# Performance work log

Hardware: AMD Instinct MI355X
Metric: run time of the kernel (lower is better)

## Reference

```python
import jax, jax.numpy as jnp
import numpy as np

H = 16  # num_attention_heads
D = 64  # attention_head_size


def setup_inputs() -> dict:
    key = jax.random.key(0)
    ks = jax.random.split(key, 10)
    B, S, Hid = 8, 512, 1024
    scale = 0.02
    hidden_states = jax.random.normal(ks[0], (B, S, Hid), jnp.float32)
    attention_mask = jnp.zeros((B, 1, 1, S), jnp.float32)
    graph_emb = jax.random.randint(ks[1], (B, S, S), 0, 3, jnp.int32)
    Wq = jax.random.normal(ks[2], (Hid, Hid), jnp.float32) * scale
    bq = jnp.zeros((Hid,), jnp.float32)
    Wk = jax.random.normal(ks[3], (Hid, Hid), jnp.float32) * scale
    bk = jnp.zeros((Hid,), jnp.float32)
    Wv = jax.random.normal(ks[4], (Hid, Hid), jnp.float32) * scale
    bv = jnp.zeros((Hid,), jnp.float32)
    dp_k = jax.random.normal(ks[5], (3, D), jnp.float32) * scale
    dp_v = jax.random.normal(ks[6], (3, D), jnp.float32) * scale
    return {"hidden_states": hidden_states, "attention_mask": attention_mask,
            "graph_emb": graph_emb, "Wq": Wq, "bq": bq, "Wk": Wk, "bk": bk,
            "Wv": Wv, "bv": bv, "dp_k": dp_k, "dp_v": dp_v}


def reference(hidden_states, attention_mask, graph_emb, Wq, bq, Wk, bk, Wv, bv, dp_k, dp_v):
    B, S, Hid = hidden_states.shape

    def proj(W, b):  # nn.Linear: x @ W.T + b, then split heads -> [B,H,S,D]
        y = hidden_states @ W.T + b
        return y.reshape(B, S, H, D).transpose(0, 2, 1, 3)

    q = proj(Wq, bq)
    k = proj(Wk, bk)
    v = proj(Wv, bv)

    # padding_idx=0 -> row 0 of relation tables is zero
    dp_k = dp_k.at[0].set(0.0)
    dp_v = dp_v.at[0].set(0.0)
    dp_keys = dp_k[graph_emb]    # [B,S,S,D]
    dp_values = dp_v[graph_emb]  # [B,S,S,D]

    scores = jnp.einsum('bhqd,bhkd->bhqk', q, k) / jnp.sqrt(jnp.float32(D))
    scores = scores + jnp.einsum('bhqd,bqkd->bhqk', q, dp_keys)  # relative_matmul_dp
    scores = scores + attention_mask
    probs = jax.nn.softmax(scores, axis=-1)

    ctx = jnp.einsum('bhqk,bhkd->bhqd', probs, v)
    ctx = ctx + jnp.einsum('bhqk,bqkd->bhqd', probs, dp_values)  # relative_matmul_dpv
    return ctx.transpose(0, 2, 1, 3).reshape(B, S, H * D)
```

## Files before the change

### kernel.cpp

```cpp
#include <hip/hip_runtime.h>
#include <hip/hip_bf16.h>
#include <cstddef>

#define B_  8
#define S_  512
#define HID 1024
#define H_  16
#define D_  64

typedef float f32x4 __attribute__((ext_vector_type(4)));
typedef _Float16 f16x8 __attribute__((ext_vector_type(8)));
typedef short s16x8 __attribute__((ext_vector_type(8)));
typedef unsigned short u16t;

__device__ __forceinline__ u16t f2h(float v) {
    return __builtin_bit_cast(u16t, (_Float16)v);
}
__device__ __forceinline__ float h2f(u16t u) {
    return (float)__builtin_bit_cast(_Float16, u);
}

__device__ __forceinline__ void gll16(const u16t* g, u16t* l) {
    __builtin_amdgcn_global_load_lds(
        (const __attribute__((address_space(1))) unsigned int*)(const void*)g,
        (__attribute__((address_space(3))) unsigned int*)(void*)l, 16, 0, 0);
}

__global__ __launch_bounds__(256) void conv_all_kernel(
    const float* __restrict__ X,
    const float* __restrict__ Wq, const float* __restrict__ Wk,
    const float* __restrict__ Wv,
    u16t* __restrict__ Xh, u16t* __restrict__ Wh)
{
    const int nX4 = (B_ * S_ * HID) / 4;
    const int nW4 = (HID * HID) / 4;
    int i = blockIdx.x * 256 + threadIdx.x;
    const float* src;
    u16t* dst;
    int off;
    if (i < nX4)                { src = X;  dst = Xh;                         off = i; }
    else if (i < nX4 + nW4)     { src = Wq; dst = Wh;                         off = i - nX4; }
    else if (i < nX4 + 2 * nW4) { src = Wk; dst = Wh + (size_t)HID * HID;     off = i - nX4 - nW4; }
    else                        { src = Wv; dst = Wh + (size_t)2 * HID * HID; off = i - nX4 - 2 * nW4; }
    float4 x = ((const float4*)src)[off];
    ushort4 h;
    h.x = f2h(x.x);
    h.y = f2h(x.y);
    h.z = f2h(x.z);
    h.w = f2h(x.w);
    ((ushort4*)dst)[off] = h;
}

__global__ __launch_bounds__(256) void qkv_mfma_kernel(
    const u16t* __restrict__ Xhi, const u16t* __restrict__ Whi,
    const float* __restrict__ bq, const float* __restrict__ bk,
    const float* __restrict__ bv,
    u16t* __restrict__ Qh, u16t* __restrict__ Kh, u16t* __restrict__ Vth)
{
    const int which = blockIdx.z;
    const u16t* __restrict__ WhiB = Whi + (size_t)which * (HID * HID);
    const float* __restrict__ bias = (which == 0) ? bq : (which == 1) ? bk : bv;

    __shared__ __align__(16) u16t SM[2 * 16384];

    const int tid  = threadIdx.x;
    const int lane = tid & 63;
    const int wv_  = tid >> 6;
    const int wr   = wv_ >> 1;
    const int wc   = wv_ & 1;
    const int m0   = blockIdx.y * 128;
    const int n0   = blockIdx.x * 128;

    f32x4 acc[4][4];
    #pragma unroll
    for (int mi = 0; mi < 4; ++mi)
        #pragma unroll
        for (int ni = 0; ni < 4; ++ni)
            #pragma unroll
            for (int e = 0; e < 4; ++e) acc[mi][ni][e] = 0.0f;

    const int rowB0 = wv_ * 32 + (lane >> 3);
    const int ch    = (lane & 7) ^ (rowB0 & 7);
    const size_t aof = (size_t)(m0 + rowB0) * HID + ch * 8;
    const size_t bof = (size_t)(n0 + rowB0) * HID + ch * 8;
    const int ldsA = (wv_ * 32) * 64;

    const int colL = lane & 15;
    const int kg   = lane >> 4;
    const int sx   = colL & 7;
    const int arow = (wr * 64 + colL) * 64;
    const int brow = (wc * 64 + colL) * 64;

    #pragma unroll
    for (int s = 0; s < 4; ++s) {
        gll16(&Xhi [aof + (size_t)(s * 8) * HID], SM + ldsA + s * 512);
        gll16(&WhiB[bof + (size_t)(s * 8) * HID], SM + 8192 + ldsA + s * 512);
    }
    __syncthreads();

    for (int k0 = 0; k0 < HID; k0 += 64) {
        const int cur = (k0 >> 6) & 1;
        u16t* const bufc = SM + cur * 16384;
        if (k0 + 64 < HID) {
            u16t* const bufn = SM + (cur ^ 1) * 16384;
            #pragma unroll
            for (int s = 0; s < 4; ++s) {
                gll16(&Xhi [aof + k0 + 64 + (size_t)(s * 8) * HID], bufn + ldsA + s * 512);
                gll16(&WhiB[bof + k0 + 64 + (size_t)(s * 8) * HID], bufn + 8192 + ldsA + s * 512);
            }
        }

        #pragma unroll
        for (int ks = 0; ks < 2; ++ks) {
            const int so = ((ks * 4 + kg) ^ sx) * 8;
            f16x8 a_[4], b_[4];
            #pragma unroll
            for (int mi = 0; mi < 4; ++mi)
                a_[mi] = *(const f16x8*)&bufc[arow + mi * 1024 + so];
            #pragma unroll
            for (int ni = 0; ni < 4; ++ni)
                b_[ni] = *(const f16x8*)&bufc[8192 + brow + ni * 1024 + so];
            #pragma unroll
            for (int mi = 0; mi < 4; ++mi)
                #pragma unroll
                for (int ni = 0; ni < 4; ++ni)
                    acc[mi][ni] = __builtin_amdgcn_mfma_f32_16x16x32_f16(
                        a_[mi], b_[ni], acc[mi][ni], 0, 0, 0);
        }
        __syncthreads();
    }

    if (which == 2) {
        #pragma unroll
        for (int mi = 0; mi < 4; ++mi) {
            #pragma unroll
            for (int ni = 0; ni < 4; ++ni) {
                const int n    = n0 + wc * 64 + ni * 16 + colL;
                const int mrow = m0 + wr * 64 + mi * 16 + kg * 4;
                const float bn = bias[n];
                const int bb = mrow >> 9;
                const int ss = mrow & (S_ - 1);
                const int hh = n >> 6;
                const int dd = n & (D_ - 1);
                ushort4 vh;
                vh.x = f2h(acc[mi][ni][0] + bn);
                vh.y = f2h(acc[mi][ni][1] + bn);
                vh.z = f2h(acc[mi][ni][2] + bn);
                vh.w = f2h(acc[mi][ni][3] + bn);
                *(ushort4*)&Vth[(((size_t)bb * H_ + hh) * D_ + dd) * S_ + ss] = vh;
            }
        }
    } else {
        u16t* __restrict__ Oh = (which == 0) ? Qh : Kh;
        float* LF = (float*)SM;
        float bn4[4];
        #pragma unroll
        for (int ni = 0; ni < 4; ++ni) bn4[ni] = bias[n0 + wc * 64 + ni * 16 + colL];

        const int er  = tid >> 3;
        const int ecc = (tid & 7) * 16;
        const int ehh = (n0 + ecc) >> 6;
        const int edd = ecc & 63;
        const int mrowE = m0 + (er >> 4) * 64 + (er & 15);

        #pragma unroll
        for (int mi = 0; mi < 4; ++mi) {
            __syncthreads();
            #pragma unroll
            for (int ni = 0; ni < 4; ++ni)
                #pragma unroll
                for (int j = 0; j < 4; ++j)
                    LF[(wr * 16 + kg * 4 + j) * 130 + wc * 64 + ni * 16 + colL] =
                        acc[mi][ni][j] + bn4[ni];
            __syncthreads();

            const int mrow = mrowE + mi * 16;
            const int bb = mrow >> 9;
            const int ss = mrow & (S_ - 1);
            __align__(16) u16t hv[16];
            #pragma unroll
            for (int u = 0; u < 16; u += 4) {
                float4 v = *(const float4*)&LF[er * 130 + ecc + u];
                hv[u + 0] = f2h(v.x);
                hv[u + 1] = f2h(v.y);
                hv[u + 2] = f2h(v.z);
                hv[u + 3] = f2h(v.w);
            }
            const size_t off = (((size_t)bb * H_ + ehh) * S_ + ss) * D_ + edd;
            *(s16x8*)&Oh[off]     = *(const s16x8*)&hv[0];
            *(s16x8*)&Oh[off + 8] = *(const s16x8*)&hv[8];
        }
    }
}

__global__ __launch_bounds__(512) void attn_mfma_kernel(
    const u16t* __restrict__ Qhg, const u16t* __restrict__ Khg,
    const u16t* __restrict__ Vhg,
    const int*  __restrict__ ge,  const float* __restrict__ mask,
    const float* __restrict__ dpk, const float* __restrict__ dpv,
    float* __restrict__ out)
{
    __shared__ __align__(16) u16t Q_s[128 * 64];
    __shared__ __align__(16) u16t K_s[64 * 64];
    __shared__ __align__(16) u16t V_s[64 * 64];
    __shared__ __align__(16) u16t P_s[8 * 2304];

    const int tid  = threadIdx.x;
    const int lane = tid & 63;
    const int wq   = tid >> 6;
    const int c    = lane & 15;
    const int g    = lane >> 4;
    const int sx   = c & 7;
    const int bid  = blockIdx.x;
    const int bh   = bid >> 2;
    const int q0   = (bid & 3) * 128;
    const int b    = bh >> 4;
    const int h    = bh & (H_ - 1);

    u16t* Pw = &P_s[wq * 2304];

    {
        const u16t* qbase = Qhg + ((size_t)bh * S_ + q0) * D_;
        #pragma unroll
        for (int t = 0; t < 2; ++t) {
            const int chk = tid + t * 512;
            const int r = chk >> 3, s = chk & 7;
            *(s16x8*)&Q_s[r * 64 + ((s ^ (r & 7)) << 3)] =
                *(const s16x8*)&qbase[chk * 8];
        }
    }

    const int r_   = tid >> 3;
    const int s_   = tid & 7;
    const int ldso = r_ * 64 + ((s_ ^ (r_ & 7)) << 3);
    const u16t* kgp = &Khg[((size_t)bh * S_ + r_) * D_ + s_ * 8];
    const u16t* vgp = &Vhg[((size_t)bh * D_ + r_) * S_ + s_ * 8];

    {
        s16x8 kr = *(const s16x8*)kgp;
        s16x8 vr = *(const s16x8*)vgp;
        *(s16x8*)&K_s[ldso] = kr;
        *(s16x8*)&V_s[ldso] = vr;
    }
    __syncthreads();

    float tq1, tq2;
    {
        const int qrow = wq * 16 + c;
        float a1 = 0.f, a2 = 0.f;
        #pragma unroll
        for (int t = 0; t < 2; ++t) {
            const int slot = 2 * g + t;
            const f16x8 qv8 = *(const f16x8*)&Q_s[qrow * 64 + ((slot ^ sx) << 3)];
            const int dbase = slot * 8;
            #pragma unroll
            for (int i = 0; i < 8; ++i) {
                const float qv = (float)qv8[i];
                a1 = fmaf(qv, dpk[D_ + dbase + i], a1);
                a2 = fmaf(qv, dpk[2 * D_ + dbase + i], a2);
            }
        }
        a1 += __shfl_xor(a1, 16); a1 += __shfl_xor(a1, 32);
        a2 += __shfl_xor(a2, 16); a2 += __shfl_xor(a2, 32);
        tq1 = a1; tq2 = a2;
    }

    const size_t geoff = ((size_t)b * S_ + q0 + wq * 16 + c) * S_;
    const float* mrow = &mask[(size_t)b * S_];

    float mrun = -INFINITY, lrun = 0.f, w1 = 0.f, w2 = 0.f;
    f32x4 ctx4[4];
    #pragma unroll
    for (int mi = 0; mi < 4; ++mi)
        #pragma unroll
        for (int e = 0; e < 4; ++e) ctx4[mi][e] = 0.f;

    for (int kt = 0; kt < S_ / 64; ++kt) {
        const int k0 = kt * 64;

        s16x8 krB, vrB;
        if (kt < S_ / 64 - 1) {
            krB = *(const s16x8*)(kgp + (size_t)(k0 + 64) * D_);
            vrB = *(const s16x8*)(vgp + (k0 + 64));
        }
        int4   gc4[4];
        float4 mk4[4];
        #pragma unroll
        for (int mi = 0; mi < 4; ++mi) {
            gc4[mi] = *(const int4*)&ge[geoff + k0 + mi * 16 + g * 4];
            mk4[mi] = *(const float4*)&mrow[k0 + mi * 16 + g * 4];
        }

        f32x4 s4[4];
        #pragma unroll
        for (int mi = 0; mi < 4; ++mi)
            #pragma unroll
            for (int e = 0; e < 4; ++e) s4[mi][e] = 0.f;

        __builtin_amdgcn_s_setprio(1);
        #pragma unroll
        for (int ks = 0; ks < 2; ++ks) {
            const int so = ((g + 4 * ks) ^ sx) << 3;
            const f16x8 qh_ = *(const f16x8*)&Q_s[(wq * 16 + c) * 64 + so];
            #pragma unroll
            for (int mi = 0; mi < 4; ++mi) {
                const f16x8 kh_ = *(const f16x8*)&K_s[(mi * 16 + c) * 64 + so];
                s4[mi] = __builtin_amdgcn_mfma_f32_16x16x32_f16(kh_, qh_, s4[mi], 0, 0, 0);
            }
        }
        __builtin_amdgcn_s_setprio(0);

        float sv[4][4];
        int   gcode[4][4];
        float tmax = -INFINITY;
        #pragma unroll
        for (int mi = 0; mi < 4; ++mi) {
            const int   gg[4] = {gc4[mi].x, gc4[mi].y, gc4[mi].z, gc4[mi].w};
            const float mm[4] = {mk4[mi].x, mk4[mi].y, mk4[mi].z, mk4[mi].w};
            #pragma unroll
            for (int j = 0; j < 4; ++j) {
                const float t = (gg[j] == 1) ? tq1 : (gg[j] == 2) ? tq2 : 0.f;
                const float x = fmaf(s4[mi][j], 0.125f, t + mm[j]);
                sv[mi][j] = x;
                gcode[mi][j] = gg[j];
                tmax = fmaxf(tmax, x);
            }
        }
        tmax = fmaxf(tmax, __shfl_xor(tmax, 16));
        tmax = fmaxf(tmax, __shfl_xor(tmax, 32));

        if (!__all(tmax - mrun <= 8.0f)) {
            const float mn    = fmaxf(mrun, tmax);
            const float alpha = __expf(mrun - mn);
            mrun = mn;
            lrun *= alpha; w1 *= alpha; w2 *= alpha;
            #pragma unroll
            for (int mi = 0; mi < 4; ++mi) ctx4[mi] *= alpha;
        }

        float rs = 0.f, rb1 = 0.f, rb2 = 0.f;
        #pragma unroll
        for (int mi = 0; mi < 4; ++mi)
            #pragma unroll
            for (int j = 0; j < 4; ++j) {
                const float e = __expf(sv[mi][j] - mrun);
                sv[mi][j] = e;
                rs += e;
                rb1 += (gcode[mi][j] == 1) ? e : 0.f;
                rb2 += (gcode[mi][j] == 2) ? e : 0.f;
            }
        rs  += __shfl_xor(rs, 16);  rs  += __shfl_xor(rs, 32);
        rb1 += __shfl_xor(rb1, 16); rb1 += __shfl_xor(rb1, 32);
        rb2 += __shfl_xor(rb2, 16); rb2 += __shfl_xor(rb2, 32);

        lrun += rs;
        w1   += rb1;
        w2   += rb2;

        #pragma unroll
        for (int mi = 0; mi < 4; ++mi) {
            ushort4 ph;
            ph.x = f2h(sv[mi][0]);
            ph.y = f2h(sv[mi][1]);
            ph.z = f2h(sv[mi][2]);
            ph.w = f2h(sv[mi][3]);
            const int slotp = (2 * mi + (g >> 1)) ^ sx;
            *(ushort4*)&Pw[c * 64 + slotp * 8 + (g & 1) * 4] = ph;
        }

        __builtin_amdgcn_s_setprio(1);
        #pragma unroll
        for (int ks = 0; ks < 2; ++ks) {
            const int so = ((g + 4 * ks) ^ sx) << 3;
            const f16x8 ph_ = *(const f16x8*)&Pw[c * 64 + so];
            #pragma unroll
            for (int mi = 0; mi < 4; ++mi) {
                const f16x8 vh_ = *(const f16x8*)&V_s[(mi * 16 + c) * 64 + so];
                ctx4[mi] = __builtin_amdgcn_mfma_f32_16x16x32_f16(vh_, ph_, ctx4[mi], 0, 0, 0);
            }
        }
        __builtin_amdgcn_s_setprio(0);
        __syncthreads();

        if (kt < S_ / 64 - 1) {
            *(s16x8*)&K_s[ldso] = krB;
            *(s16x8*)&V_s[ldso] = vrB;
            __syncthreads();
        }
    }

    const float inv = 1.0f / lrun;
    float* tb = (float*)&P_s[wq * 2304];
    #pragma unroll
    for (int mi = 0; mi < 4; ++mi) {
        const float4 dk1 = *(const float4*)&dpv[D_ + mi * 16 + g * 4];
        const float4 dk2 = *(const float4*)&dpv[2 * D_ + mi * 16 + g * 4];
        const float a1[4] = {dk1.x, dk1.y, dk1.z, dk1.w};
        const float a2[4] = {dk2.x, dk2.y, dk2.z, dk2.w};
        #pragma unroll
        for (int j = 0; j < 4; ++j) {
            const float val = (ctx4[mi][j] + w1 * a1[j] + w2 * a2[j]) * inv;
            tb[(mi * 16 + g * 4 + j) * 17 + c] = val;
        }
    }
    __syncthreads();
    #pragma unroll
    for (int qq = 0; qq < 16; ++qq)
        out[((size_t)b * S_ + q0 + wq * 16 + qq) * (H_ * D_) + h * D_ + lane] =
            tb[lane * 17 + qq];
}

extern "C" void kernel_launch(void* const* d_in, const int* in_sizes, int n_in,
                              void* d_out, int out_size, void* d_ws, size_t ws_size,
                              hipStream_t stream)
{
    const float* hs   = (const float*)d_in[0];
    const float* mask = (const float*)d_in[1];
    const int*   ge   = (const int*)d_in[2];
    const float* Wq   = (const float*)d_in[3];
    const float* bq   = (const float*)d_in[4];
    const float* Wk   = (const float*)d_in[5];
    const float* bk   = (const float*)d_in[6];
    const float* Wv   = (const float*)d_in[7];
    const float* bv   = (const float*)d_in[8];
    const float* dpk  = (const float*)d_in[9];
    const float* dpv  = (const float*)d_in[10];
    float* out = (float*)d_out;

    const size_t per = (size_t)B_ * H_ * S_ * D_;
    const size_t nX  = (size_t)B_ * S_ * HID;
    const size_t nW  = (size_t)HID * HID;

    u16t* base = (u16t*)d_ws;
    u16t* Qh  = base;
    u16t* Kh  = Qh  + per;
    u16t* Vth = Kh  + per;
    u16t* Xhi = Vth + per;
    u16t* Whi = Xhi + nX;

    const int nConv = (int)((nX + 3 * nW) / 4);
    conv_all_kernel<<<nConv / 256, 256, 0, stream>>>(hs, Wq, Wk, Wv, Xhi, Whi);

    dim3 gridG(HID / 128, (B_ * S_) / 128, 3);
    qkv_mfma_kernel<<<gridG, dim3(256), 0, stream>>>(
        Xhi, Whi, bq, bk, bv, Qh, Kh, Vth);

    dim3 gridB(B_ * H_ * (S_ / 128));
    attn_mfma_kernel<<<gridB, dim3(512), 0, stream>>>(
        Qh, Kh, Vth, ge, mask, dpk, dpv, out);
}
```

Before: 79.65 us.

## Keep Q in registers and double-buffer K/V tiles with one barrier per step

Q fragments are loaded straight from global memory into registers, so the Q tile no longer needs to be staged in LDS. K/V tiles are now double-buffered in a single shared array. Each iteration stores the prefetched tile into the alternate buffer before one __syncthreads, instead of a trailing barrier plus a store and a second barrier. Per-wave P scratch shrinks and LDS use drops substantially, which may allow more resident blocks per CU, at the cost of some extra registers for the held Q fragments.

```diff
diff --git a/kernel.cpp b/kernel.cpp
--- a/kernel.cpp
+++ b/kernel.cpp
@@ -200,10 +200,7 @@
     const float* __restrict__ dpk, const float* __restrict__ dpv,
     float* __restrict__ out)
 {
-    __shared__ __align__(16) u16t Q_s[128 * 64];
-    __shared__ __align__(16) u16t K_s[64 * 64];
-    __shared__ __align__(16) u16t V_s[64 * 64];
-    __shared__ __align__(16) u16t P_s[8 * 2304];
+    __shared__ __align__(16) u16t SM[24576];
 
     const int tid  = threadIdx.x;
     const int lane = tid & 63;
@@ -217,17 +214,28 @@
     const int b    = bh >> 4;
     const int h    = bh & (H_ - 1);
 
-    u16t* Pw = &P_s[wq * 2304];
-
+    u16t* Pw = SM + 16384 + wq * 1024;
+
+    const int qrow = q0 + wq * 16 + c;
+    const size_t qoff = ((size_t)bh * S_ + qrow) * D_;
+    const f16x8 qA = *(const f16x8*)&Qhg[qoff + g * 8];
+    const f16x8 qB = *(const f16x8*)&Qhg[qoff + (g + 4) * 8];
+
+    float tq1, tq2;
     {
-        const u16t* qbase = Qhg + ((size_t)bh * S_ + q0) * D_;
-        #pragma unroll
-        for (int t = 0; t < 2; ++t) {
-            const int chk = tid + t * 512;
-            const int r = chk >> 3, s = chk & 7;
-            *(s16x8*)&Q_s[r * 64 + ((s ^ (r & 7)) << 3)] =
-                *(const s16x8*)&qbase[chk * 8];
-        }
+        float a1 = 0.f, a2 = 0.f;
+        #pragma unroll
+        for (int i = 0; i < 8; ++i) {
+            const float x0 = (float)qA[i];
+            const float x1 = (float)qB[i];
+            a1 = fmaf(x0, dpk[D_ + g * 8 + i], a1);
+            a1 = fmaf(x1, dpk[D_ + (g + 4) * 8 + i], a1);
+            a2 = fmaf(x0, dpk[2 * D_ + g * 8 + i], a2);
+            a2 = fmaf(x1, dpk[2 * D_ + (g + 4) * 8 + i], a2);
+        }
+        a1 += __shfl_xor(a1, 16); a1 += __shfl_xor(a1, 32);
+        a2 += __shfl_xor(a2, 16); a2 += __shfl_xor(a2, 32);
+        tq1 = a1; tq2 = a2;
     }
 
     const int r_   = tid >> 3;
@@ -236,36 +244,10 @@
     const u16t* kgp = &Khg[((size_t)bh * S_ + r_) * D_ + s_ * 8];
     const u16t* vgp = &Vhg[((size_t)bh * D_ + r_) * S_ + s_ * 8];
 
-    {
-        s16x8 kr = *(const s16x8*)kgp;
-        s16x8 vr = *(const s16x8*)vgp;
-        *(s16x8*)&K_s[ldso] = kr;
-        *(s16x8*)&V_s[ldso] = vr;
-    }
-    __syncthreads();
-
-    float tq1, tq2;
-    {
-        const int qrow = wq * 16 + c;
-        float a1 = 0.f, a2 = 0.f;
-        #pragma unroll
-        for (int t = 0; t < 2; ++t) {
-            const int slot = 2 * g + t;
-            const f16x8 qv8 = *(const f16x8*)&Q_s[qrow * 64 + ((slot ^ sx) << 3)];
-            const int dbase = slot * 8;
-            #pragma unroll
-            for (int i = 0; i < 8; ++i) {
-                const float qv = (float)qv8[i];
-                a1 = fmaf(qv, dpk[D_ + dbase + i], a1);
-                a2 = fmaf(qv, dpk[2 * D_ + dbase + i], a2);
-            }
-        }
-        a1 += __shfl_xor(a1, 16); a1 += __shfl_xor(a1, 32);
-        a2 += __shfl_xor(a2, 16); a2 += __shfl_xor(a2, 32);
-        tq1 = a1; tq2 = a2;
-    }
-
-    const size_t geoff = ((size_t)b * S_ + q0 + wq * 16 + c) * S_;
+    s16x8 krS = *(const s16x8*)kgp;
+    s16x8 vrS = *(const s16x8*)vgp;
+
+    const size_t geoff = ((size_t)b * S_ + qrow) * S_;
     const float* mrow = &mask[(size_t)b * S_];
 
     float mrun = -INFINITY, lrun = 0.f, w1 = 0.f, w2 = 0.f;
@@ -277,11 +259,16 @@
 
     for (int kt = 0; kt < S_ / 64; ++kt) {
         const int k0 = kt * 64;
-
-        s16x8 krB, vrB;
+        const int bufo = (kt & 1) << 13;
+        u16t* const Kb = SM + bufo;
+        u16t* const Vb = SM + bufo + 4096;
+
+        *(s16x8*)&Kb[ldso] = krS;
+        *(s16x8*)&Vb[ldso] = vrS;
+
         if (kt < S_ / 64 - 1) {
-            krB = *(const s16x8*)(kgp + (size_t)(k0 + 64) * D_);
-            vrB = *(const s16x8*)(vgp + (k0 + 64));
+            krS = *(const s16x8*)(kgp + (size_t)(k0 + 64) * D_);
+            vrS = *(const s16x8*)(vgp + (k0 + 64));
         }
         int4   gc4[4];
         float4 mk4[4];
@@ -291,6 +278,8 @@
             mk4[mi] = *(const float4*)&mrow[k0 + mi * 16 + g * 4];
         }
 
+        __syncthreads();
+
         f32x4 s4[4];
         #pragma unroll
         for (int mi = 0; mi < 4; ++mi)
@@ -301,10 +290,10 @@
         #pragma unroll
         for (int ks = 0; ks < 2; ++ks) {
             const int so = ((g + 4 * ks) ^ sx) << 3;
-            const f16x8 qh_ = *(const f16x8*)&Q_s[(wq * 16 + c) * 64 + so];
+            const f16x8 qh_ = ks ? qB : qA;
             #pragma unroll
             for (int mi = 0; mi < 4; ++mi) {
-                const f16x8 kh_ = *(const f16x8*)&K_s[(mi * 16 + c) * 64 + so];
+                const f16x8 kh_ = *(const f16x8*)&Kb[(mi * 16 + c) * 64 + so];
                 s4[mi] = __builtin_amdgcn_mfma_f32_16x16x32_f16(kh_, qh_, s4[mi], 0, 0, 0);
             }
         }
@@ -375,22 +364,16 @@
             const f16x8 ph_ = *(const f16x8*)&Pw[c * 64 + so];
             #pragma unroll
             for (int mi = 0; mi < 4; ++mi) {
-                const f16x8 vh_ = *(const f16x8*)&V_s[(mi * 16 + c) * 64 + so];
+                const f16x8 vh_ = *(const f16x8*)&Vb[(mi * 16 + c) * 64 + so];
                 ctx4[mi] = __builtin_amdgcn_mfma_f32_16x16x32_f16(vh_, ph_, ctx4[mi], 0, 0, 0);
             }
         }
         __builtin_amdgcn_s_setprio(0);
-        __syncthreads();
-
-        if (kt < S_ / 64 - 1) {
-            *(s16x8*)&K_s[ldso] = krB;
-            *(s16x8*)&V_s[ldso] = vrB;
-            __syncthreads();
-        }
-    }
-
+    }
+
+    __syncthreads();
     const float inv = 1.0f / lrun;
-    float* tb = (float*)&P_s[wq * 2304];
+    float* tb = (float*)SM + wq * 1088;
     #pragma unroll
     for (int mi = 0; mi < 4; ++mi) {
         const float4 dk1 = *(const float4*)&dpv[D_ + mi * 16 + g * 4];
```

Result: faster. 78.02 us (-2.0%).
